# Performance work log

Measured on AMD Instinct MI355X. Metric: run time of the kernel, lower is better.

## Reference

```python
import jax, jax.numpy as jnp
import numpy as np
import math

NUM_CLUSTERS = 196
NBH = 10          # find_nearest_minima neighborhood_size
MAX_ITER = 2
M_WEIGHT = 10.0   # SLIC m


def _grid_centroids(C, H, W):
    # place_centroids_on_grid (static, python ints -> faithful int() truncation)
    num_cols = int(math.sqrt(C * W / H))
    num_rows = int(math.ceil(C / num_cols))
    gy, gx = H / num_rows, W / num_cols
    pts = []
    for i in range(num_rows):
        for j in range(num_cols):
            if len(pts) >= C:
                break
            pts.append([int((i + 0.5) * gy), int((j + 0.5) * gx)])
        if len(pts) >= C:
            break
    return np.asarray(pts, np.int32)


def _find_minima(g, cents):
    # g: [H,W] grad map, cents: [C,2] int. Sequential collision-avoiding move of
    # each centroid to the first unoccupied argmin of its (2*NBH)^2 window,
    # exactly matching the torch row-major tie iteration + occupied set.
    H, W = g.shape
    yy = jnp.arange(H)[:, None]
    xx = jnp.arange(W)[None, :]

    def step(occ, c):
        cy, cx = c[0], c[1]
        wm = (yy >= cy - NBH) & (yy < cy + NBH) & (xx >= cx - NBH) & (xx < cx + NBH)
        mval = jnp.min(jnp.where(wm, g, jnp.inf))
        avail = wm & (g == mval) & (~occ)
        found = jnp.any(avail)
        idx = jnp.argmax(avail.reshape(-1))  # first True in row-major order
        ny = (idx // W).astype(c.dtype)
        nx = (idx % W).astype(c.dtype)
        newc = jnp.where(found, jnp.stack([ny, nx]), c)
        occ = jnp.where(found, occ.at[ny, nx].set(True), occ)
        return occ, newc

    _, out = jax.lax.scan(step, jnp.zeros((H, W), dtype=bool), cents)
    return out  # [C,2] int


def _slic(x, cents):
    # x: [B,Cin,H,W], cents: [B,C,2] int (y,x). Returns label map [B,H,W].
    B, Cin, H, W = x.shape
    C = cents.shape[1]
    S = int(math.sqrt(H * W / C) + 0.5)
    yc, xc = cents[..., 0], cents[..., 1]

    # initial centroid colors = x at (clamped) centroid positions
    xf = x.reshape(B, Cin, H * W)

    def gather_colors(xb, ycb, xcb):
        idx = jnp.clip(ycb, 0, H - 1) * W + jnp.clip(xcb, 0, W - 1)
        return xb[:, idx].T  # [C,Cin]

    colors = jax.vmap(gather_colors)(xf, yc, xc)  # [B,C,Cin]

    yi = jnp.arange(H)
    xi = jnp.arange(W)
    x2 = jnp.sum(x * x, axis=1)  # [B,H,W]
    pix = jnp.arange(H * W)
    yidx = (pix // W).astype(jnp.float32)
    xidx = (pix % W).astype(jnp.float32)
    xp = x.transpose(0, 2, 3, 1).reshape(B, H * W, Cin)  # pixel colors

    lbl = jnp.full((B, H, W), -1)
    for _ in range(MAX_ITER):
        # color distance ||x_p - col_c|| via gram expansion: [B,C,H,W]
        c2 = jnp.sum(colors * colors, axis=-1)  # [B,C]
        cross = jnp.einsum('bchw,bkc->bkhw', x, colors)
        cd = jnp.sqrt(jnp.maximum(x2[:, None] + c2[:, :, None, None] - 2.0 * cross, 0.0))
        # spatial distance (separable pieces broadcast to [B,C,H,W])
        dy = yi[None, None, :].astype(jnp.float32) - yc[:, :, None].astype(jnp.float32)  # [B,C,H]
        dx = xi[None, None, :].astype(jnp.float32) - xc[:, :, None].astype(jnp.float32)  # [B,C,W]
        sp = jnp.sqrt(dy[:, :, :, None] ** 2 + dx[:, :, None, :] ** 2)
        # 2S x 2S window mask == torch slice [max(0,c-S), min(HW,c+S))
        ym = (yi[None, None, :] >= (yc - S)[:, :, None]) & (yi[None, None, :] < (yc + S)[:, :, None])
        xm = (xi[None, None, :] >= (xc - S)[:, :, None]) & (xi[None, None, :] < (xc + S)[:, :, None])
        dist = jnp.where(ym[:, :, :, None] & xm[:, :, None, :], cd + (M_WEIGHT / S) * sp, jnp.inf)
        # sequential strict-> update == first-argmin over clusters
        mind = jnp.min(dist, axis=1)
        lbl = jnp.where(jnp.isfinite(mind), jnp.argmin(dist, axis=1), -1)  # [B,H,W]

        # centroid update: per-cluster mean position / color via segment_sum
        seg = jnp.where(lbl < 0, C, lbl).reshape(B, H * W)

        def upd(segb, xpb):
            ones = jnp.ones(H * W, jnp.float32)
            cnt = jax.ops.segment_sum(ones, segb, num_segments=C + 1)[:C]
            sy = jax.ops.segment_sum(yidx, segb, num_segments=C + 1)[:C]
            sx = jax.ops.segment_sum(xidx, segb, num_segments=C + 1)[:C]
            sc = jax.ops.segment_sum(xpb, segb, num_segments=C + 1)[:C]
            return cnt, sy, sx, sc

        cnt, sy, sx, sc = jax.vmap(upd)(seg, xp)
        has = cnt > 0
        denom = jnp.maximum(cnt, 1.0)
        yc = jnp.where(has, jnp.round(jnp.clip(sy / denom, 0, H - 1)).astype(yc.dtype), yc)
        xc = jnp.where(has, jnp.round(jnp.clip(sx / denom, 0, W - 1)).astype(xc.dtype), xc)
        colors = jnp.where(has[..., None], sc / denom[..., None], colors)
    return lbl


def setup_inputs() -> dict:
    key = jax.random.key(0)
    k1, k2 = jax.random.split(key)
    x = jax.random.normal(k1, (8, 3, 224, 224), dtype=jnp.float32)
    grad_map = jax.random.uniform(k2, (8, 1, 224, 224), dtype=jnp.float32)
    return {"x": x, "grad_map": grad_map}


def reference(x, grad_map):
    g = grad_map[:, 0]  # [B,H,W]
    H, W = g.shape[1], g.shape[2]
    cents0 = jnp.asarray(_grid_centroids(NUM_CLUSTERS, H, W))
    cents = jax.vmap(lambda gb: _find_minima(gb, cents0))(g)  # [B,C,2]
    mask = _slic(x, cents)  # [B,H,W]
    return cents.astype(jnp.float32), mask
```

## Files before the change

### kernel.cpp

```cpp
#include <hip/hip_runtime.h>
#include <math.h>

#define HH 224
#define WW 224
#define BB 8
#define NC 196
#define NBHD 10
#define SS 16
#define MW_OVER_S 0.625f

__global__ void k_window_scan(const float* __restrict__ g,
                              float* __restrict__ wmin,
                              int* __restrict__ widx,
                              int* __restrict__ wcnt) {
    int c = blockIdx.x, b = blockIdx.y;
    int lane = threadIdx.x;
    const float* gb = g + b * HH * WW;
    int gy = 8 + 16 * (c / 14), gx = 8 + 16 * (c % 14);
    int y0 = max(0, gy - NBHD), y1 = min(HH, gy + NBHD);
    int x0 = max(0, gx - NBHD), x1 = min(WW, gx + NBHD);
    int wd = x1 - x0;
    int n = (y1 - y0) * wd;

    float m = INFINITY;
    for (int i = lane; i < n; i += 64) {
        int y = y0 + i / wd, x = x0 + i % wd;
        m = fminf(m, gb[y * WW + x]);
    }
    for (int off = 1; off < 64; off <<= 1)
        m = fminf(m, __shfl_xor(m, off));

    int bidx = 0x7fffffff;
    int cnt = 0;
    for (int i = lane; i < n; i += 64) {
        int y = y0 + i / wd, x = x0 + i % wd;
        int f = y * WW + x;
        if (gb[f] == m) { bidx = min(bidx, f); ++cnt; }
    }
    for (int off = 1; off < 64; off <<= 1) {
        bidx = min(bidx, __shfl_xor(bidx, off));
        cnt += __shfl_xor(cnt, off);
    }
    if (lane == 0) {
        wmin[b * NC + c] = m;
        widx[b * NC + c] = bidx;
        wcnt[b * NC + c] = cnt;
    }
}

__global__ void k_resolve(const float* __restrict__ g,
                          const float* __restrict__ x,
                          const float* __restrict__ wmin,
                          const int* __restrict__ widx,
                          const int* __restrict__ wcnt,
                          int* __restrict__ yc, int* __restrict__ xc,
                          float* __restrict__ colors,
                          float* __restrict__ out_cents) {
    __shared__ int s_idx[NC];
    __shared__ int s_cnt[NC];
    __shared__ float s_minv[NC];
    __shared__ unsigned char occ[HH * WW];
    int b = blockIdx.x, lane = threadIdx.x;
    const float* gb = g + b * HH * WW;
    const float* xb = x + b * 3 * HH * WW;

    for (int i = lane; i < NC; i += 64) {
        s_idx[i] = widx[b * NC + i];
        s_cnt[i] = wcnt[b * NC + i];
        s_minv[i] = wmin[b * NC + i];
    }
    __syncthreads();

    bool tie = false;
    for (int i = lane; i < NC; i += 64) tie |= (s_cnt[i] > 1);
    if (!__any(tie)) {
        for (int c = lane; c < NC; c += 64) {
            int idx = s_idx[c];
            int row = c / 14, col = c % 14;
            bool bumped = (col > 0 && s_idx[c - 1] == idx);
            if (row > 0) {
                bumped |= (s_idx[c - 14] == idx);
                if (col > 0)  bumped |= (s_idx[c - 15] == idx);
                if (col < 13) bumped |= (s_idx[c - 13] == idx);
            }
            int ny, nx;
            if (bumped) { ny = 8 + 16 * row; nx = 8 + 16 * col; }
            else        { ny = idx / WW;     nx = idx % WW;     }
            yc[b * NC + c] = ny; xc[b * NC + c] = nx;
            out_cents[(b * NC + c) * 2 + 0] = (float)ny;
            out_cents[(b * NC + c) * 2 + 1] = (float)nx;
            int p = ny * WW + nx;
            colors[(b * NC + c) * 3 + 0] = xb[p];
            colors[(b * NC + c) * 3 + 1] = xb[HH * WW + p];
            colors[(b * NC + c) * 3 + 2] = xb[2 * HH * WW + p];
        }
        return;
    }

    unsigned int* occ32 = (unsigned int*)occ;
    for (int i = lane; i < (HH * WW) / 4; i += 64) occ32[i] = 0u;
    __syncthreads();

    for (int c = 0; c < NC; ++c) {
        int idx = s_idx[c];
        int cnt = s_cnt[c];
        bool occd = (occ[idx] != 0);
        int chosen;
        if (cnt == 1) {
            chosen = occd ? -1 : idx;
        } else if (!occd) {
            chosen = idx;
        } else {
            float m = s_minv[c];
            int gy = 8 + 16 * (c / 14), gx = 8 + 16 * (c % 14);
            int wy0 = max(0, gy - NBHD), wy1 = min(HH, gy + NBHD);
            int wx0 = max(0, gx - NBHD), wx1 = min(WW, gx + NBHD);
            int wd = wx1 - wx0;
            int n = (wy1 - wy0) * wd;
            int best = 0x7fffffff;
            for (int i = lane; i < n; i += 64) {
                int y = wy0 + i / wd, xx = wx0 + i % wd;
                int f = y * WW + xx;
                if (gb[f] == m && !occ[f]) best = min(best, f);
            }
            for (int off = 1; off < 64; off <<= 1)
                best = min(best, __shfl_xor(best, off));
            chosen = (best == 0x7fffffff) ? -1 : best;
        }
        int ny, nx;
        if (chosen >= 0) {
            ny = chosen / WW; nx = chosen % WW;
            if (lane == 0) occ[chosen] = 1;
        } else {
            ny = 8 + 16 * (c / 14); nx = 8 + 16 * (c % 14);
        }
        if (lane == 0) {
            yc[b * NC + c] = ny;
            xc[b * NC + c] = nx;
            out_cents[(b * NC + c) * 2 + 0] = (float)ny;
            out_cents[(b * NC + c) * 2 + 1] = (float)nx;
        }
        __syncthreads();
    }
    for (int k = lane; k < NC; k += 64) {
        int y = yc[b * NC + k], xx = xc[b * NC + k];
        int idx = y * WW + xx;
        colors[(b * NC + k) * 3 + 0] = xb[idx];
        colors[(b * NC + k) * 3 + 1] = xb[HH * WW + idx];
        colors[(b * NC + k) * 3 + 2] = xb[2 * HH * WW + idx];
    }
}

__global__ void k_assign(const float* __restrict__ x,
                         const int* __restrict__ yc,
                         const int* __restrict__ xc,
                         const float* __restrict__ colors,
                         float* __restrict__ lblf) {
    __shared__ int s_yc[NC], s_xc[NC];
    __shared__ float s_c0[NC], s_c1[NC], s_c2[NC], s_cc[NC];
    __shared__ int s_cand[NC];
    __shared__ int s_wc[4];
    int b = blockIdx.z;
    int ty0 = blockIdx.y * 16, tx0 = blockIdx.x * 16;
    int t = threadIdx.y * 16 + threadIdx.x;
    int lane = t & 63, wid = t >> 6;

    bool pred = false;
    if (t < NC) {
        int yck = yc[b * NC + t], xck = xc[b * NC + t];
        s_yc[t] = yck; s_xc[t] = xck;
        float c0 = colors[(b * NC + t) * 3 + 0];
        float c1 = colors[(b * NC + t) * 3 + 1];
        float c2 = colors[(b * NC + t) * 3 + 2];
        s_c0[t] = c0; s_c1[t] = c1; s_c2[t] = c2;
        s_cc[t] = __fadd_rn(__fadd_rn(__fmul_rn(c0, c0), __fmul_rn(c1, c1)), __fmul_rn(c2, c2));
        pred = (yck > ty0 - 17 && yck < ty0 + 32 && xck > tx0 - 17 && xck < tx0 + 32);
    }
    unsigned long long bm = __ballot(pred);
    if (lane == 0) s_wc[wid] = __popcll(bm);
    __syncthreads();
    int base = 0;
    for (int w = 0; w < wid; ++w) base += s_wc[w];
    if (pred) {
        int pos = base + __popcll(bm & ((1ull << lane) - 1ull));
        s_cand[pos] = t;
    }
    int n = s_wc[0] + s_wc[1] + s_wc[2] + s_wc[3];
    __syncthreads();

    int h = ty0 + threadIdx.y, w = tx0 + threadIdx.x;
    const float* xb = x + b * 3 * HH * WW;
    int pidx = h * WW + w;
    float x0v = xb[pidx];
    float x1v = xb[HH * WW + pidx];
    float x2v = xb[2 * HH * WW + pidx];
    float px2 = __fadd_rn(__fadd_rn(__fmul_rn(x0v, x0v), __fmul_rn(x1v, x1v)), __fmul_rn(x2v, x2v));
    float hf = (float)h, wf = (float)w;

    float best = INFINITY;
    int bestk = -1;
    for (int i = 0; i < n; ++i) {
        int k = s_cand[i];
        int yck = s_yc[k], xck = s_xc[k];
        if (h >= yck - SS && h < yck + SS && w >= xck - SS && w < xck + SS) {
            float cross = __fadd_rn(__fadd_rn(__fmul_rn(x0v, s_c0[k]), __fmul_rn(x1v, s_c1[k])),
                                    __fmul_rn(x2v, s_c2[k]));
            float t2 = __fsub_rn(__fadd_rn(px2, s_cc[k]), __fmul_rn(2.0f, cross));
            float cd = __fsqrt_rn(fmaxf(t2, 0.0f));
            float dy = __fsub_rn(hf, (float)yck);
            float dx = __fsub_rn(wf, (float)xck);
            float sp = __fsqrt_rn(__fadd_rn(__fmul_rn(dy, dy), __fmul_rn(dx, dx)));
            float d = __fadd_rn(cd, __fmul_rn(MW_OVER_S, sp));
            if (d < best || (d == best && k < bestk)) { best = d; bestk = k; }
        }
    }
    lblf[b * HH * WW + pidx] = (float)bestk;
}

__global__ void k_update(const float* __restrict__ x,
                         const float* __restrict__ lblf,
                         int* __restrict__ yc, int* __restrict__ xc,
                         float* __restrict__ colors) {
    __shared__ alignas(16) float sc0[1024];
    __shared__ alignas(16) float sc1[1024];
    __shared__ alignas(16) float sc2[1024];
    __shared__ int wsum[4];
    __shared__ int s_isy, s_isx;
    __shared__ float s_fin[3];
    int k = blockIdx.x, b = blockIdx.y;
    int t = threadIdx.x;
    int lane = t & 63, wid = t >> 6;

    int yck = yc[b * NC + k], xck = xc[b * NC + k];
    int y0 = max(0, yck - SS), y1 = min(HH, yck + SS);
    int x0 = max(0, xck - SS), x1 = min(WW, xck + SS);
    int wd = x1 - x0;
    int n = (y1 - y0) * wd;

    const float* xb = x + b * 3 * HH * WW;
    const float* lb = lblf + b * HH * WW;
    float kf = (float)k;

    if (t == 0) { s_isy = 0; s_isx = 0; }
    __syncthreads();

    int mask = 0;
    int isy = 0, isx = 0;
    #pragma unroll
    for (int j = 0; j < 4; ++j) {
        int i = 4 * t + j;
        if (i < n) {
            int y = y0 + i / wd, xx = x0 + i % wd;
            if (lb[y * WW + xx] == kf) { mask |= (1 << j); isy += y; isx += xx; }
        }
    }
    int c_t = __popc(mask);

    int inc = c_t;
    for (int off = 1; off < 64; off <<= 1) {
        int u = __shfl_up(inc, off);
        if (lane >= off) inc += u;
    }
    if (lane == 63) wsum[wid] = inc;
    __syncthreads();
    int woff = 0;
    for (int w = 0; w < wid; ++w) woff += wsum[w];
    int pos = woff + inc - c_t;

    #pragma unroll
    for (int j = 0; j < 4; ++j) {
        if ((mask >> j) & 1) {
            int i = 4 * t + j;
            int y = y0 + i / wd, xx = x0 + i % wd;
            int idx = y * WW + xx;
            sc0[pos] = xb[idx];
            sc1[pos] = xb[HH * WW + idx];
            sc2[pos] = xb[2 * HH * WW + idx];
            ++pos;
        }
    }
    for (int off = 1; off < 64; off <<= 1) {
        isy += __shfl_xor(isy, off);
        isx += __shfl_xor(isx, off);
    }
    if (lane == 0) { atomicAdd(&s_isy, isy); atomicAdd(&s_isx, isx); }
    __syncthreads();

    int cnt = wsum[0] + wsum[1] + wsum[2] + wsum[3];

    if (t < 3) {
        const float* a = (t == 0) ? sc0 : (t == 1) ? sc1 : sc2;
        float s = 0.0f;
        int i = 0;
        for (; i + 8 <= cnt; i += 8) {
            float4 q0 = *(const float4*)(a + i);
            float4 q1 = *(const float4*)(a + i + 4);
            s = __fadd_rn(s, q0.x); s = __fadd_rn(s, q0.y);
            s = __fadd_rn(s, q0.z); s = __fadd_rn(s, q0.w);
            s = __fadd_rn(s, q1.x); s = __fadd_rn(s, q1.y);
            s = __fadd_rn(s, q1.z); s = __fadd_rn(s, q1.w);
        }
        for (; i < cnt; ++i) s = __fadd_rn(s, a[i]);
        s_fin[t] = s;
    }
    __syncthreads();

    if (t == 0 && cnt > 0) {
        float denom = (float)cnt;
        float nyf = rintf(fminf(fmaxf(__fdiv_rn((float)s_isy, denom), 0.0f), (float)(HH - 1)));
        float nxf = rintf(fminf(fmaxf(__fdiv_rn((float)s_isx, denom), 0.0f), (float)(WW - 1)));
        yc[b * NC + k] = (int)nyf;
        xc[b * NC + k] = (int)nxf;
        colors[(b * NC + k) * 3 + 0] = __fdiv_rn(s_fin[0], denom);
        colors[(b * NC + k) * 3 + 1] = __fdiv_rn(s_fin[1], denom);
        colors[(b * NC + k) * 3 + 2] = __fdiv_rn(s_fin[2], denom);
    }
}

extern "C" void kernel_launch(void* const* d_in, const int* in_sizes, int n_in,
                              void* d_out, int out_size, void* d_ws, size_t ws_size,
                              hipStream_t stream) {
    const float* x = (const float*)d_in[0];
    const float* g = (const float*)d_in[1];
    float* out = (float*)d_out;
    float* out_cents = out;
    float* lblf = out + BB * NC * 2;

    int* yc = (int*)d_ws;
    int* xc = yc + BB * NC;
    float* colors = (float*)(xc + BB * NC);
    float* wmin = colors + BB * NC * 3;
    int* widx = (int*)(wmin + BB * NC);
    int* wcnt = widx + BB * NC;

    dim3 gscan(NC, BB);
    k_window_scan<<<gscan, 64, 0, stream>>>(g, wmin, widx, wcnt);
    k_resolve<<<BB, 64, 0, stream>>>(g, x, wmin, widx, wcnt, yc, xc, colors, out_cents);

    dim3 gridA(WW / 16, HH / 16, BB);
    dim3 blkA(16, 16);
    dim3 gupd(NC, BB);
    k_assign<<<gridA, blkA, 0, stream>>>(x, yc, xc, colors, lblf);
    k_update<<<gupd, 256, 0, stream>>>(x, lblf, yc, xc, colors);
    k_assign<<<gridA, blkA, 0, stream>>>(x, yc, xc, colors, lblf);
}
```

Before: 93.93 us.

## Fuse window scan into resolve kernel and move occupancy map to global workspace

Removes the separate window-scan kernel. Each resolve block, now 1024 threads, has its 16 wavefronts scan the 196 centroid windows directly and keep the results in shared memory. The occupancy map moves from 50KB of LDS to a per-batch global workspace with volatile access and threadfences, so a large block fits. This drops one launch and the global round-trip for the scan results, but the scan now runs on only 8 blocks instead of 1568, which cuts parallelism for that phase.

```diff
diff --git a/kernel.cpp b/kernel.cpp
--- a/kernel.cpp
+++ b/kernel.cpp
@@ -9,72 +9,64 @@
 #define SS 16
 #define MW_OVER_S 0.625f
 
-__global__ void k_window_scan(const float* __restrict__ g,
-                              float* __restrict__ wmin,
-                              int* __restrict__ widx,
-                              int* __restrict__ wcnt) {
-    int c = blockIdx.x, b = blockIdx.y;
-    int lane = threadIdx.x;
-    const float* gb = g + b * HH * WW;
-    int gy = 8 + 16 * (c / 14), gx = 8 + 16 * (c % 14);
-    int y0 = max(0, gy - NBHD), y1 = min(HH, gy + NBHD);
-    int x0 = max(0, gx - NBHD), x1 = min(WW, gx + NBHD);
-    int wd = x1 - x0;
-    int n = (y1 - y0) * wd;
-
-    float m = INFINITY;
-    for (int i = lane; i < n; i += 64) {
-        int y = y0 + i / wd, x = x0 + i % wd;
-        m = fminf(m, gb[y * WW + x]);
-    }
-    for (int off = 1; off < 64; off <<= 1)
-        m = fminf(m, __shfl_xor(m, off));
-
-    int bidx = 0x7fffffff;
-    int cnt = 0;
-    for (int i = lane; i < n; i += 64) {
-        int y = y0 + i / wd, x = x0 + i % wd;
-        int f = y * WW + x;
-        if (gb[f] == m) { bidx = min(bidx, f); ++cnt; }
-    }
-    for (int off = 1; off < 64; off <<= 1) {
-        bidx = min(bidx, __shfl_xor(bidx, off));
-        cnt += __shfl_xor(cnt, off);
-    }
-    if (lane == 0) {
-        wmin[b * NC + c] = m;
-        widx[b * NC + c] = bidx;
-        wcnt[b * NC + c] = cnt;
-    }
-}
-
 __global__ void k_resolve(const float* __restrict__ g,
                           const float* __restrict__ x,
-                          const float* __restrict__ wmin,
-                          const int* __restrict__ widx,
-                          const int* __restrict__ wcnt,
                           int* __restrict__ yc, int* __restrict__ xc,
                           float* __restrict__ colors,
-                          float* __restrict__ out_cents) {
+                          float* __restrict__ out_cents,
+                          unsigned char* __restrict__ occ_ws) {
     __shared__ int s_idx[NC];
     __shared__ int s_cnt[NC];
     __shared__ float s_minv[NC];
-    __shared__ unsigned char occ[HH * WW];
-    int b = blockIdx.x, lane = threadIdx.x;
+    __shared__ int s_tie;
+    int b = blockIdx.x;
+    int t = threadIdx.x;
+    int lane = t & 63, wv = t >> 6;
     const float* gb = g + b * HH * WW;
     const float* xb = x + b * 3 * HH * WW;
 
-    for (int i = lane; i < NC; i += 64) {
-        s_idx[i] = widx[b * NC + i];
-        s_cnt[i] = wcnt[b * NC + i];
-        s_minv[i] = wmin[b * NC + i];
-    }
-    __syncthreads();
-
-    bool tie = false;
-    for (int i = lane; i < NC; i += 64) tie |= (s_cnt[i] > 1);
-    if (!__any(tie)) {
-        for (int c = lane; c < NC; c += 64) {
+    if (t == 0) s_tie = 0;
+
+    for (int c = wv; c < NC; c += 16) {
+        int gy = 8 + 16 * (c / 14), gx = 8 + 16 * (c % 14);
+        int y0 = max(0, gy - NBHD), y1 = min(HH, gy + NBHD);
+        int x0 = max(0, gx - NBHD), x1 = min(WW, gx + NBHD);
+        int wd = x1 - x0;
+        int n = (y1 - y0) * wd;
+
+        float m = INFINITY;
+        for (int i = lane; i < n; i += 64) {
+            int y = y0 + i / wd, xx = x0 + i % wd;
+            m = fminf(m, gb[y * WW + xx]);
+        }
+        for (int off = 1; off < 64; off <<= 1)
+            m = fminf(m, __shfl_xor(m, off));
+
+        int bidx = 0x7fffffff;
+        int cnt = 0;
+        for (int i = lane; i < n; i += 64) {
+            int y = y0 + i / wd, xx = x0 + i % wd;
+            int f = y * WW + xx;
+            if (gb[f] == m) { bidx = min(bidx, f); ++cnt; }
+        }
+        for (int off = 1; off < 64; off <<= 1) {
+            bidx = min(bidx, __shfl_xor(bidx, off));
+            cnt += __shfl_xor(cnt, off);
+        }
+        if (lane == 0) {
+            s_minv[c] = m;
+            s_idx[c] = bidx;
+            s_cnt[c] = cnt;
+        }
+    }
+    __syncthreads();
+
+    if (t < NC && s_cnt[t] > 1) s_tie = 1;
+    __syncthreads();
+
+    if (!s_tie) {
+        if (t < NC) {
+            int c = t;
             int idx = s_idx[c];
             int row = c / 14, col = c % 14;
             bool bumped = (col > 0 && s_idx[c - 1] == idx);
@@ -97,57 +89,62 @@
         return;
     }
 
+    unsigned char* occ = occ_ws + b * HH * WW;
+    volatile unsigned char* occv = occ;
     unsigned int* occ32 = (unsigned int*)occ;
-    for (int i = lane; i < (HH * WW) / 4; i += 64) occ32[i] = 0u;
+    for (int i = t; i < (HH * WW) / 4; i += 1024) occ32[i] = 0u;
+    __threadfence();
     __syncthreads();
 
     for (int c = 0; c < NC; ++c) {
-        int idx = s_idx[c];
-        int cnt = s_cnt[c];
-        bool occd = (occ[idx] != 0);
-        int chosen;
-        if (cnt == 1) {
-            chosen = occd ? -1 : idx;
-        } else if (!occd) {
-            chosen = idx;
-        } else {
-            float m = s_minv[c];
-            int gy = 8 + 16 * (c / 14), gx = 8 + 16 * (c % 14);
-            int wy0 = max(0, gy - NBHD), wy1 = min(HH, gy + NBHD);
-            int wx0 = max(0, gx - NBHD), wx1 = min(WW, gx + NBHD);
-            int wd = wx1 - wx0;
-            int n = (wy1 - wy0) * wd;
-            int best = 0x7fffffff;
-            for (int i = lane; i < n; i += 64) {
-                int y = wy0 + i / wd, xx = wx0 + i % wd;
-                int f = y * WW + xx;
-                if (gb[f] == m && !occ[f]) best = min(best, f);
+        int chosen = -2;
+        if (t < 64) {
+            int idx = s_idx[c];
+            int cnt = s_cnt[c];
+            bool occd = (occv[idx] != 0);
+            if (cnt == 1) {
+                chosen = occd ? -1 : idx;
+            } else if (!occd) {
+                chosen = idx;
+            } else {
+                float m = s_minv[c];
+                int gy = 8 + 16 * (c / 14), gx = 8 + 16 * (c % 14);
+                int wy0 = max(0, gy - NBHD), wy1 = min(HH, gy + NBHD);
+                int wx0 = max(0, gx - NBHD), wx1 = min(WW, gx + NBHD);
+                int wd = wx1 - wx0;
+                int n = (wy1 - wy0) * wd;
+                int best = 0x7fffffff;
+                for (int i = lane; i < n; i += 64) {
+                    int y = wy0 + i / wd, xx = wx0 + i % wd;
+                    int f = y * WW + xx;
+                    if (gb[f] == m && !occv[f]) best = min(best, f);
+                }
+                for (int off = 1; off < 64; off <<= 1)
+                    best = min(best, __shfl_xor(best, off));
+                chosen = (best == 0x7fffffff) ? -1 : best;
             }
-            for (int off = 1; off < 64; off <<= 1)
-                best = min(best, __shfl_xor(best, off));
-            chosen = (best == 0x7fffffff) ? -1 : best;
-        }
-        int ny, nx;
-        if (chosen >= 0) {
-            ny = chosen / WW; nx = chosen % WW;
-            if (lane == 0) occ[chosen] = 1;
-        } else {
-            ny = 8 + 16 * (c / 14); nx = 8 + 16 * (c % 14);
-        }
-        if (lane == 0) {
-            yc[b * NC + c] = ny;
-            xc[b * NC + c] = nx;
-            out_cents[(b * NC + c) * 2 + 0] = (float)ny;
-            out_cents[(b * NC + c) * 2 + 1] = (float)nx;
+            int ny, nx;
+            if (chosen >= 0) {
+                ny = chosen / WW; nx = chosen % WW;
+                if (t == 0) { occ[chosen] = 1; __threadfence(); }
+            } else {
+                ny = 8 + 16 * (c / 14); nx = 8 + 16 * (c % 14);
+            }
+            if (t == 0) {
+                yc[b * NC + c] = ny;
+                xc[b * NC + c] = nx;
+                out_cents[(b * NC + c) * 2 + 0] = (float)ny;
+                out_cents[(b * NC + c) * 2 + 1] = (float)nx;
+            }
         }
         __syncthreads();
     }
-    for (int k = lane; k < NC; k += 64) {
-        int y = yc[b * NC + k], xx = xc[b * NC + k];
+    if (t < NC) {
+        int y = yc[b * NC + t], xx = xc[b * NC + t];
         int idx = y * WW + xx;
-        colors[(b * NC + k) * 3 + 0] = xb[idx];
-        colors[(b * NC + k) * 3 + 1] = xb[HH * WW + idx];
-        colors[(b * NC + k) * 3 + 2] = xb[2 * HH * WW + idx];
+        colors[(b * NC + t) * 3 + 0] = xb[idx];
+        colors[(b * NC + t) * 3 + 1] = xb[HH * WW + idx];
+        colors[(b * NC + t) * 3 + 2] = xb[2 * HH * WW + idx];
     }
 }
 
@@ -329,13 +326,9 @@
     int* yc = (int*)d_ws;
     int* xc = yc + BB * NC;
     float* colors = (float*)(xc + BB * NC);
-    float* wmin = colors + BB * NC * 3;
-    int* widx = (int*)(wmin + BB * NC);
-    int* wcnt = widx + BB * NC;
-
-    dim3 gscan(NC, BB);
-    k_window_scan<<<gscan, 64, 0, stream>>>(g, wmin, widx, wcnt);
-    k_resolve<<<BB, 64, 0, stream>>>(g, x, wmin, widx, wcnt, yc, xc, colors, out_cents);
+    unsigned char* occ_ws = (unsigned char*)(colors + BB * NC * 3);
+
+    k_resolve<<<BB, 1024, 0, stream>>>(g, x, yc, xc, colors, out_cents, occ_ws);
 
     dim3 gridA(WW / 16, HH / 16, BB);
     dim3 blkA(16, 16);
```

After: 144.1 us. +53.4%, slower.

## Fuse centroid resolve into first assignment kernel, recomputed per tile

Applied to the files above, without the earlier changes.

Removes the separate per-batch resolve kernel and folds its work into the first assignment kernel. Each 16x16 tile block now redundantly recomputes the centroid positions and colors in shared memory, and only tile (0,0) writes them to global memory. The tie path uses a bit-packed occupancy map and a 256-thread block reduction. This saves one launch and a serial 8-block kernel, at the cost of redundant per-block work and a much larger shared-memory footprint in the assign kernel, which may lower occupancy.

```diff
diff --git a/kernel.cpp b/kernel.cpp
--- a/kernel.cpp
+++ b/kernel.cpp
@@ -48,132 +48,125 @@
     }
 }
 
-__global__ void k_resolve(const float* __restrict__ g,
-                          const float* __restrict__ x,
-                          const float* __restrict__ wmin,
-                          const int* __restrict__ widx,
-                          const int* __restrict__ wcnt,
-                          int* __restrict__ yc, int* __restrict__ xc,
-                          float* __restrict__ colors,
-                          float* __restrict__ out_cents) {
-    __shared__ int s_idx[NC];
-    __shared__ int s_cnt[NC];
+__global__ void k_assign_first(const float* __restrict__ g,
+                               const float* __restrict__ x,
+                               const int* __restrict__ widx,
+                               const int* __restrict__ wcnt,
+                               const float* __restrict__ wmin,
+                               int* __restrict__ yc, int* __restrict__ xc,
+                               float* __restrict__ colors,
+                               float* __restrict__ out_cents,
+                               float* __restrict__ lblf) {
+    __shared__ int s_idx[NC], s_cnt[NC];
     __shared__ float s_minv[NC];
-    __shared__ unsigned char occ[HH * WW];
-    int b = blockIdx.x, lane = threadIdx.x;
+    __shared__ int s_yc[NC], s_xc[NC];
+    __shared__ float s_c0[NC], s_c1[NC], s_c2[NC], s_cc[NC];
+    __shared__ int s_cand[NC];
+    __shared__ int s_wc[4];
+    __shared__ int s_tie;
+    __shared__ int s_bmin[4];
+    __shared__ unsigned int occbits[(HH * WW + 31) / 32];
+    int b = blockIdx.z;
+    int ty0 = blockIdx.y * 16, tx0 = blockIdx.x * 16;
+    int t = threadIdx.y * 16 + threadIdx.x;
+    int lane = t & 63, wid = t >> 6;
     const float* gb = g + b * HH * WW;
     const float* xb = x + b * 3 * HH * WW;
 
-    for (int i = lane; i < NC; i += 64) {
-        s_idx[i] = widx[b * NC + i];
-        s_cnt[i] = wcnt[b * NC + i];
-        s_minv[i] = wmin[b * NC + i];
-    }
-    __syncthreads();
-
-    bool tie = false;
-    for (int i = lane; i < NC; i += 64) tie |= (s_cnt[i] > 1);
-    if (!__any(tie)) {
-        for (int c = lane; c < NC; c += 64) {
-            int idx = s_idx[c];
-            int row = c / 14, col = c % 14;
-            bool bumped = (col > 0 && s_idx[c - 1] == idx);
+    if (t == 0) s_tie = 0;
+    if (t < NC) {
+        s_idx[t] = widx[b * NC + t];
+        s_cnt[t] = wcnt[b * NC + t];
+        s_minv[t] = wmin[b * NC + t];
+    }
+    __syncthreads();
+    if (t < NC && s_cnt[t] > 1) s_tie = 1;
+    __syncthreads();
+
+    if (!s_tie) {
+        if (t < NC) {
+            int idx = s_idx[t];
+            int row = t / 14, col = t % 14;
+            bool bumped = (col > 0 && s_idx[t - 1] == idx);
             if (row > 0) {
-                bumped |= (s_idx[c - 14] == idx);
-                if (col > 0)  bumped |= (s_idx[c - 15] == idx);
-                if (col < 13) bumped |= (s_idx[c - 13] == idx);
+                bumped |= (s_idx[t - 14] == idx);
+                if (col > 0)  bumped |= (s_idx[t - 15] == idx);
+                if (col < 13) bumped |= (s_idx[t - 13] == idx);
             }
             int ny, nx;
             if (bumped) { ny = 8 + 16 * row; nx = 8 + 16 * col; }
             else        { ny = idx / WW;     nx = idx % WW;     }
-            yc[b * NC + c] = ny; xc[b * NC + c] = nx;
-            out_cents[(b * NC + c) * 2 + 0] = (float)ny;
-            out_cents[(b * NC + c) * 2 + 1] = (float)nx;
-            int p = ny * WW + nx;
-            colors[(b * NC + c) * 3 + 0] = xb[p];
-            colors[(b * NC + c) * 3 + 1] = xb[HH * WW + p];
-            colors[(b * NC + c) * 3 + 2] = xb[2 * HH * WW + p];
-        }
-        return;
-    }
-
-    unsigned int* occ32 = (unsigned int*)occ;
-    for (int i = lane; i < (HH * WW) / 4; i += 64) occ32[i] = 0u;
-    __syncthreads();
-
-    for (int c = 0; c < NC; ++c) {
-        int idx = s_idx[c];
-        int cnt = s_cnt[c];
-        bool occd = (occ[idx] != 0);
-        int chosen;
-        if (cnt == 1) {
-            chosen = occd ? -1 : idx;
-        } else if (!occd) {
-            chosen = idx;
-        } else {
-            float m = s_minv[c];
-            int gy = 8 + 16 * (c / 14), gx = 8 + 16 * (c % 14);
-            int wy0 = max(0, gy - NBHD), wy1 = min(HH, gy + NBHD);
-            int wx0 = max(0, gx - NBHD), wx1 = min(WW, gx + NBHD);
-            int wd = wx1 - wx0;
-            int n = (wy1 - wy0) * wd;
-            int best = 0x7fffffff;
-            for (int i = lane; i < n; i += 64) {
-                int y = wy0 + i / wd, xx = wx0 + i % wd;
-                int f = y * WW + xx;
-                if (gb[f] == m && !occ[f]) best = min(best, f);
+            s_yc[t] = ny; s_xc[t] = nx;
+        }
+    } else {
+        for (int i = t; i < (HH * WW + 31) / 32; i += 256) occbits[i] = 0u;
+        __syncthreads();
+        for (int c = 0; c < NC; ++c) {
+            int idx = s_idx[c];
+            int cnt = s_cnt[c];
+            bool occd = (occbits[idx >> 5] >> (idx & 31)) & 1;
+            int chosen;
+            if (cnt == 1) {
+                chosen = occd ? -1 : idx;
+            } else if (!occd) {
+                chosen = idx;
+            } else {
+                float m = s_minv[c];
+                int gy = 8 + 16 * (c / 14), gx = 8 + 16 * (c % 14);
+                int wy0 = max(0, gy - NBHD), wy1 = min(HH, gy + NBHD);
+                int wx0 = max(0, gx - NBHD), wx1 = min(WW, gx + NBHD);
+                int wdw = wx1 - wx0;
+                int nn = (wy1 - wy0) * wdw;
+                int best = 0x7fffffff;
+                for (int i = t; i < nn; i += 256) {
+                    int y = wy0 + i / wdw, xx2 = wx0 + i % wdw;
+                    int f = y * WW + xx2;
+                    bool o = (occbits[f >> 5] >> (f & 31)) & 1;
+                    if (gb[f] == m && !o) best = min(best, f);
+                }
+                for (int off = 1; off < 64; off <<= 1)
+                    best = min(best, __shfl_xor(best, off));
+                if (lane == 0) s_bmin[wid] = best;
+                __syncthreads();
+                best = min(min(s_bmin[0], s_bmin[1]), min(s_bmin[2], s_bmin[3]));
+                chosen = (best == 0x7fffffff) ? -1 : best;
             }
-            for (int off = 1; off < 64; off <<= 1)
-                best = min(best, __shfl_xor(best, off));
-            chosen = (best == 0x7fffffff) ? -1 : best;
-        }
-        int ny, nx;
-        if (chosen >= 0) {
-            ny = chosen / WW; nx = chosen % WW;
-            if (lane == 0) occ[chosen] = 1;
-        } else {
-            ny = 8 + 16 * (c / 14); nx = 8 + 16 * (c % 14);
-        }
-        if (lane == 0) {
-            yc[b * NC + c] = ny;
-            xc[b * NC + c] = nx;
-            out_cents[(b * NC + c) * 2 + 0] = (float)ny;
-            out_cents[(b * NC + c) * 2 + 1] = (float)nx;
-        }
-        __syncthreads();
-    }
-    for (int k = lane; k < NC; k += 64) {
-        int y = yc[b * NC + k], xx = xc[b * NC + k];
-        int idx = y * WW + xx;
-        colors[(b * NC + k) * 3 + 0] = xb[idx];
-        colors[(b * NC + k) * 3 + 1] = xb[HH * WW + idx];
-        colors[(b * NC + k) * 3 + 2] = xb[2 * HH * WW + idx];
-    }
-}
-
-__global__ void k_assign(const float* __restrict__ x,
-                         const int* __restrict__ yc,
-                         const int* __restrict__ xc,
-                         const float* __restrict__ colors,
-                         float* __restrict__ lblf) {
-    __shared__ int s_yc[NC], s_xc[NC];
-    __shared__ float s_c0[NC], s_c1[NC], s_c2[NC], s_cc[NC];
-    __shared__ int s_cand[NC];
-    __shared__ int s_wc[4];
-    int b = blockIdx.z;
-    int ty0 = blockIdx.y * 16, tx0 = blockIdx.x * 16;
-    int t = threadIdx.y * 16 + threadIdx.x;
-    int lane = t & 63, wid = t >> 6;
+            if (t == 0) {
+                int ny, nx;
+                if (chosen >= 0) {
+                    ny = chosen / WW; nx = chosen % WW;
+                    occbits[chosen >> 5] |= (1u << (chosen & 31));
+                } else {
+                    ny = 8 + 16 * (c / 14); nx = 8 + 16 * (c % 14);
+                }
+                s_yc[c] = ny; s_xc[c] = nx;
+            }
+            __syncthreads();
+        }
+    }
+    __syncthreads();
+
+    if (t < NC) {
+        int p = s_yc[t] * WW + s_xc[t];
+        float c0 = xb[p];
+        float c1 = xb[HH * WW + p];
+        float c2 = xb[2 * HH * WW + p];
+        s_c0[t] = c0; s_c1[t] = c1; s_c2[t] = c2;
+        s_cc[t] = __fadd_rn(__fadd_rn(__fmul_rn(c0, c0), __fmul_rn(c1, c1)), __fmul_rn(c2, c2));
+        if (blockIdx.x == 0 && blockIdx.y == 0) {
+            yc[b * NC + t] = s_yc[t];
+            xc[b * NC + t] = s_xc[t];
+            out_cents[(b * NC + t) * 2 + 0] = (float)s_yc[t];
+            out_cents[(b * NC + t) * 2 + 1] = (float)s_xc[t];
+            colors[(b * NC + t) * 3 + 0] = c0;
+            colors[(b * NC + t) * 3 + 1] = c1;
+            colors[(b * NC + t) * 3 + 2] = c2;
+        }
+    }
 
     bool pred = false;
     if (t < NC) {
-        int yck = yc[b * NC + t], xck = xc[b * NC + t];
-        s_yc[t] = yck; s_xc[t] = xck;
-        float c0 = colors[(b * NC + t) * 3 + 0];
-        float c1 = colors[(b * NC + t) * 3 + 1];
-        float c2 = colors[(b * NC + t) * 3 + 2];
-        s_c0[t] = c0; s_c1[t] = c1; s_c2[t] = c2;
-        s_cc[t] = __fadd_rn(__fadd_rn(__fmul_rn(c0, c0), __fmul_rn(c1, c1)), __fmul_rn(c2, c2));
+        int yck = s_yc[t], xck = s_xc[t];
         pred = (yck > ty0 - 17 && yck < ty0 + 32 && xck > tx0 - 17 && xck < tx0 + 32);
     }
     unsigned long long bm = __ballot(pred);
@@ -189,7 +182,6 @@
     __syncthreads();
 
     int h = ty0 + threadIdx.y, w = tx0 + threadIdx.x;
-    const float* xb = x + b * 3 * HH * WW;
     int pidx = h * WW + w;
     float x0v = xb[pidx];
     float x1v = xb[HH * WW + pidx];
@@ -217,6 +209,72 @@
     lblf[b * HH * WW + pidx] = (float)bestk;
 }
 
+__global__ void k_assign(const float* __restrict__ x,
+                         const int* __restrict__ yc,
+                         const int* __restrict__ xc,
+                         const float* __restrict__ colors,
+                         float* __restrict__ lblf) {
+    __shared__ int s_yc[NC], s_xc[NC];
+    __shared__ float s_c0[NC], s_c1[NC], s_c2[NC], s_cc[NC];
+    __shared__ int s_cand[NC];
+    __shared__ int s_wc[4];
+    int b = blockIdx.z;
+    int ty0 = blockIdx.y * 16, tx0 = blockIdx.x * 16;
+    int t = threadIdx.y * 16 + threadIdx.x;
+    int lane = t & 63, wid = t >> 6;
+
+    bool pred = false;
+    if (t < NC) {
+        int yck = yc[b * NC + t], xck = xc[b * NC + t];
+        s_yc[t] = yck; s_xc[t] = xck;
+        float c0 = colors[(b * NC + t) * 3 + 0];
+        float c1 = colors[(b * NC + t) * 3 + 1];
+        float c2 = colors[(b * NC + t) * 3 + 2];
+        s_c0[t] = c0; s_c1[t] = c1; s_c2[t] = c2;
+        s_cc[t] = __fadd_rn(__fadd_rn(__fmul_rn(c0, c0), __fmul_rn(c1, c1)), __fmul_rn(c2, c2));
+        pred = (yck > ty0 - 17 && yck < ty0 + 32 && xck > tx0 - 17 && xck < tx0 + 32);
+    }
+    unsigned long long bm = __ballot(pred);
+    if (lane == 0) s_wc[wid] = __popcll(bm);
+    __syncthreads();
+    int base = 0;
+    for (int w = 0; w < wid; ++w) base += s_wc[w];
+    if (pred) {
+        int pos = base + __popcll(bm & ((1ull << lane) - 1ull));
+        s_cand[pos] = t;
+    }
+    int n = s_wc[0] + s_wc[1] + s_wc[2] + s_wc[3];
+    __syncthreads();
+
+    int h = ty0 + threadIdx.y, w = tx0 + threadIdx.x;
+    const float* xb = x + b * 3 * HH * WW;
+    int pidx = h * WW + w;
+    float x0v = xb[pidx];
+    float x1v = xb[HH * WW + pidx];
+    float x2v = xb[2 * HH * WW + pidx];
+    float px2 = __fadd_rn(__fadd_rn(__fmul_rn(x0v, x0v), __fmul_rn(x1v, x1v)), __fmul_rn(x2v, x2v));
+    float hf = (float)h, wf = (float)w;
+
+    float best = INFINITY;
+    int bestk = -1;
+    for (int i = 0; i < n; ++i) {
+        int k = s_cand[i];
+        int yck = s_yc[k], xck = s_xc[k];
+        if (h >= yck - SS && h < yck + SS && w >= xck - SS && w < xck + SS) {
+            float cross = __fadd_rn(__fadd_rn(__fmul_rn(x0v, s_c0[k]), __fmul_rn(x1v, s_c1[k])),
+                                    __fmul_rn(x2v, s_c2[k]));
+            float t2 = __fsub_rn(__fadd_rn(px2, s_cc[k]), __fmul_rn(2.0f, cross));
+            float cd = __fsqrt_rn(fmaxf(t2, 0.0f));
+            float dy = __fsub_rn(hf, (float)yck);
+            float dx = __fsub_rn(wf, (float)xck);
+            float sp = __fsqrt_rn(__fadd_rn(__fmul_rn(dy, dy), __fmul_rn(dx, dx)));
+            float d = __fadd_rn(cd, __fmul_rn(MW_OVER_S, sp));
+            if (d < best || (d == best && k < bestk)) { best = d; bestk = k; }
+        }
+    }
+    lblf[b * HH * WW + pidx] = (float)bestk;
+}
+
 __global__ void k_update(const float* __restrict__ x,
                          const float* __restrict__ lblf,
                          int* __restrict__ yc, int* __restrict__ xc,
@@ -335,12 +393,12 @@
 
     dim3 gscan(NC, BB);
     k_window_scan<<<gscan, 64, 0, stream>>>(g, wmin, widx, wcnt);
-    k_resolve<<<BB, 64, 0, stream>>>(g, x, wmin, widx, wcnt, yc, xc, colors, out_cents);
 
     dim3 gridA(WW / 16, HH / 16, BB);
     dim3 blkA(16, 16);
     dim3 gupd(NC, BB);
-    k_assign<<<gridA, blkA, 0, stream>>>(x, yc, xc, colors, lblf);
+    k_assign_first<<<gridA, blkA, 0, stream>>>(g, x, widx, wcnt, wmin,
+                                               yc, xc, colors, out_cents, lblf);
     k_update<<<gupd, 256, 0, stream>>>(x, lblf, yc, xc, colors);
     k_assign<<<gridA, blkA, 0, stream>>>(x, yc, xc, colors, lblf);
 }
```

Result: no change. 92.52 us (-1.5%).
